# Kernel optimization log

Measured on AMD Instinct MI355X. Metric: run time of the kernel, lower is better.

The kernel has to match this reference:

```python
import jax, jax.numpy as jnp
import numpy as np

N = 50000      # nodes
E = 800000     # edges
F_IN = 500     # input features
H = 128        # hidden_channels
C = 10         # classes


def setup_inputs() -> dict:
    key = jax.random.key(0)
    ks = jax.random.split(key, 9)
    x = jax.random.normal(ks[0], (N, F_IN), dtype=jnp.float32)
    edge_index = jax.random.randint(ks[1], (2, E), 0, N, dtype=jnp.int32)
    W1 = jax.random.normal(ks[2], (F_IN, H), dtype=jnp.float32) * 0.05
    b1 = jnp.zeros((H,), dtype=jnp.float32)
    W2 = jax.random.normal(ks[3], (H, H), dtype=jnp.float32) * 0.05
    b2 = jnp.zeros((H,), dtype=jnp.float32)
    Wo = jax.random.normal(ks[4], (H, C), dtype=jnp.float32) * 0.05
    bo = jnp.zeros((C,), dtype=jnp.float32)
    return {"x": x, "edge_index": edge_index, "W1": W1, "b1": b1,
            "W2": W2, "b2": b2, "Wo": Wo, "bo": bo}


def _gcn_conv(x, src, dst, norm, W, b):
    # x: [N, F] -> [N, out]; PyG GCNConv: transform, then normalized scatter-add
    h = x @ W                                    # [N, out]
    msg = h[src] * norm[:, None]                 # [E+N, out] gathered messages
    agg = jax.ops.segment_sum(msg, dst, num_segments=N)
    return agg + b


def reference(x, edge_index, W1, b1, W2, b2, Wo, bo):
    loop = jnp.arange(N, dtype=edge_index.dtype)
    src = jnp.concatenate([edge_index[0], loop])  # add self-loops
    dst = jnp.concatenate([edge_index[1], loop])
    # symmetric normalization deg^-1/2 A_hat deg^-1/2 (deg counted at target)
    deg = jnp.zeros((N,), dtype=x.dtype).at[dst].add(1.0)
    dis = jnp.where(deg > 0, jax.lax.rsqrt(deg), 0.0)
    norm = dis[src] * dis[dst]

    h = jax.nn.relu(_gcn_conv(x, src, dst, norm, W1, b1))
    h = jax.nn.relu(_gcn_conv(h, src, dst, norm, W2, b2))
    # eval-mode: dropout is identity
    return jax.nn.softmax(h @ Wo + bo, axis=1)
```

## Files before the change

### kernel.cpp

```cpp
#include <hip/hip_runtime.h>
#include <hip/hip_bf16.h>
#include <stdint.h>

#define N_NODES 50000
#define N_EDGES 800000
#define F_IN    500
#define HID     128
#define NCLS    10

typedef __attribute__((ext_vector_type(8))) short bf16x8;
typedef __attribute__((ext_vector_type(4))) float f32x4;


__global__ __launch_bounds__(256) void count_deg_k(const int* dst, int* cnt) {
    int e = blockIdx.x * 256 + threadIdx.x;
    if (e < N_EDGES) atomicAdd(&cnt[dst[e]], 1);
}

__global__ __launch_bounds__(256) void compute_dis_k(const int* cnt, float* dis) {
    int i = blockIdx.x * 256 + threadIdx.x;
    if (i < N_NODES) {
        float deg = (float)(cnt[i] + 1);
        dis[i] = rsqrtf(deg);
    }
}

__global__ __launch_bounds__(1024) void scan_k(const int* __restrict__ cnt, int* __restrict__ off) {
    __shared__ int part[1024];
    const int PER = 52;
    int tid = threadIdx.x;
    int base = tid * PER;
    int vals[PER];
    #pragma unroll
    for (int i = 0; i < PER; i += 4) {
        int idx = base + i;
        int4 v = make_int4(0, 0, 0, 0);
        if (idx + 3 < N_NODES) {
            v = *(const int4*)&cnt[idx];
        } else {
            if (idx + 0 < N_NODES) v.x = cnt[idx + 0];
            if (idx + 1 < N_NODES) v.y = cnt[idx + 1];
            if (idx + 2 < N_NODES) v.z = cnt[idx + 2];
            if (idx + 3 < N_NODES) v.w = cnt[idx + 3];
        }
        vals[i + 0] = v.x; vals[i + 1] = v.y; vals[i + 2] = v.z; vals[i + 3] = v.w;
    }
    int s = 0;
    #pragma unroll
    for (int i = 0; i < PER; ++i) s += vals[i];
    part[tid] = s;
    __syncthreads();
    for (int o = 1; o < 1024; o <<= 1) {
        int v = (tid >= o) ? part[tid - o] : 0;
        __syncthreads();
        part[tid] += v;
        __syncthreads();
    }
    int run = part[tid] - s;
    #pragma unroll
    for (int i = 0; i < PER; ++i) {
        int idx = base + i;
        if (idx < N_NODES) { off[idx] = run; run += vals[i]; }
    }
    if (tid == 1023) off[N_NODES] = N_EDGES;
}

__global__ __launch_bounds__(256) void fill_csr_k(const int* src, const int* dst,
                                                  const int* off, int* cur, int* csr) {
    int e = blockIdx.x * 256 + threadIdx.x;
    if (e < N_EDGES) {
        int d = dst[e];
        int p = off[d] + atomicAdd(&cur[d], 1);
        csr[p] = src[e];
    }
}


__global__ __launch_bounds__(256) void transpose_cast_k(const float* __restrict__ W,
                                                        __hip_bfloat16* __restrict__ WT,
                                                        int K, int KPAD) {
    int id = blockIdx.x * 256 + threadIdx.x;
    if (id >= 128 * KPAD) return;
    int n = id / KPAD;
    int k = id - n * KPAD;
    WT[id] = (k < K) ? __float2bfloat16(W[(long)k * 128 + n]) : __float2bfloat16(0.f);
}


template<int KPAD, int KREAL>
__global__ __launch_bounds__(256) void gemm_mfma_k(const float* __restrict__ A,
                                                   const __hip_bfloat16* __restrict__ BT,
                                                   float* __restrict__ Out, int M) {
    __shared__ __hip_bfloat16 As[64][72];
    __shared__ __hip_bfloat16 Bs[128][72];
    const int tid  = threadIdx.x;
    const int row0 = blockIdx.x * 64;
    const int wid  = tid >> 6, lane = tid & 63;
    const int wr   = (wid >> 1) * 32;
    const int wc   = (wid & 1) * 64;
    const int l15  = lane & 15;
    const int lk   = (lane >> 4) * 8;

    f32x4 acc[2][4];
    #pragma unroll
    for (int i = 0; i < 2; ++i)
        #pragma unroll
        for (int j = 0; j < 4; ++j) acc[i][j] = (f32x4){0.f, 0.f, 0.f, 0.f};

    const int arow = tid >> 2;
    const int aseg = (tid & 3) * 16;
    const int brow = tid >> 1;
    const int bseg = (tid & 1) * 32;
    const bool rowok = (row0 + arow) < M;
    const float* aptr = A + (long)(row0 + arow) * KREAL;

    for (int k0 = 0; k0 < KPAD; k0 += 64) {
        {
            float v[16];
            const float* ap = aptr + k0 + aseg;
            if (rowok && (k0 + aseg + 16 <= KREAL)) {
                #pragma unroll
                for (int i = 0; i < 4; ++i) {
                    float4 f = ((const float4*)ap)[i];
                    v[i*4+0] = f.x; v[i*4+1] = f.y; v[i*4+2] = f.z; v[i*4+3] = f.w;
                }
            } else {
                #pragma unroll
                for (int i = 0; i < 16; ++i) {
                    int gk = k0 + aseg + i;
                    v[i] = (rowok && gk < KREAL) ? ap[i] : 0.f;
                }
            }
            __hip_bfloat16 bb[16];
            #pragma unroll
            for (int i = 0; i < 16; ++i) bb[i] = __float2bfloat16(v[i]);
            *(bf16x8*)&As[arow][aseg]     = *(bf16x8*)&bb[0];
            *(bf16x8*)&As[arow][aseg + 8] = *(bf16x8*)&bb[8];
        }
        {
            const __hip_bfloat16* bp = BT + (long)brow * KPAD + k0 + bseg;
            #pragma unroll
            for (int i = 0; i < 4; ++i)
                *(bf16x8*)&Bs[brow][bseg + i * 8] = ((const bf16x8*)bp)[i];
        }
        __syncthreads();
        #pragma unroll
        for (int kk = 0; kk < 64; kk += 32) {
            bf16x8 af[2], bfr[4];
            #pragma unroll
            for (int i = 0; i < 2; ++i)
                af[i] = *(const bf16x8*)&As[wr + i * 16 + l15][kk + lk];
            #pragma unroll
            for (int j = 0; j < 4; ++j)
                bfr[j] = *(const bf16x8*)&Bs[wc + j * 16 + l15][kk + lk];
            #pragma unroll
            for (int i = 0; i < 2; ++i)
                #pragma unroll
                for (int j = 0; j < 4; ++j)
                    acc[i][j] = __builtin_amdgcn_mfma_f32_16x16x32_bf16(af[i], bfr[j], acc[i][j], 0, 0, 0);
        }
        __syncthreads();
    }
    const int r4 = (lane >> 4) * 4;
    #pragma unroll
    for (int i = 0; i < 2; ++i) {
        #pragma unroll
        for (int r = 0; r < 4; ++r) {
            int grow = row0 + wr + i * 16 + r4 + r;
            if (grow < M) {
                float* op = Out + (long)grow * 128 + wc + l15;
                #pragma unroll
                for (int j = 0; j < 4; ++j) op[j * 16] = acc[i][j][r];
            }
        }
    }
}


__global__ __launch_bounds__(256) void agg_k(const float* __restrict__ Hin,
                                             float* __restrict__ Hout,
                                             const int* __restrict__ off,
                                             const int* __restrict__ csr,
                                             const float* __restrict__ dis,
                                             const float* __restrict__ bias) {
    int w = (blockIdx.x * 256 + threadIdx.x) >> 6;
    int lane = threadIdx.x & 63;
    if (w >= N_NODES) return;
    int n = w;
    int e0 = off[n], e1 = off[n + 1];
    float dn = dis[n];

    const float2* hn = (const float2*)(Hin + (long)n * HID);
    float2 hv = hn[lane];
    float sw = dn * dn;
    float ax = hv.x * sw, ay = hv.y * sw;

    int e = e0;
    for (; e + 4 <= e1; e += 4) {
        int s0 = csr[e + 0], s1 = csr[e + 1], s2 = csr[e + 2], s3 = csr[e + 3];
        float w0 = dis[s0] * dn, w1 = dis[s1] * dn, w2 = dis[s2] * dn, w3 = dis[s3] * dn;
        float2 m0 = ((const float2*)(Hin + (long)s0 * HID))[lane];
        float2 m1 = ((const float2*)(Hin + (long)s1 * HID))[lane];
        float2 m2 = ((const float2*)(Hin + (long)s2 * HID))[lane];
        float2 m3 = ((const float2*)(Hin + (long)s3 * HID))[lane];
        ax = fmaf(m0.x, w0, ax); ay = fmaf(m0.y, w0, ay);
        ax = fmaf(m1.x, w1, ax); ay = fmaf(m1.y, w1, ay);
        ax = fmaf(m2.x, w2, ax); ay = fmaf(m2.y, w2, ay);
        ax = fmaf(m3.x, w3, ax); ay = fmaf(m3.y, w3, ay);
    }
    for (; e < e1; ++e) {
        int s = csr[e];
        float wgt = dis[s] * dn;
        float2 m = ((const float2*)(Hin + (long)s * HID))[lane];
        ax = fmaf(m.x, wgt, ax);
        ay = fmaf(m.y, wgt, ay);
    }
    float2 bv = ((const float2*)bias)[lane];
    float ox = ax + bv.x, oy = ay + bv.y;
    ox = ox > 0.f ? ox : 0.f;
    oy = oy > 0.f ? oy : 0.f;
    ((float2*)(Hout + (long)n * HID))[lane] = make_float2(ox, oy);
}


__global__ __launch_bounds__(256) void head_k(const float* __restrict__ Hf,
                                              const float* __restrict__ Wo,
                                              const float* __restrict__ bo,
                                              float* __restrict__ out) {
    __shared__ float wsh[HID * NCLS];
    __shared__ float bsh[NCLS];
    int tid = threadIdx.x;
    for (int i = tid; i < HID * NCLS; i += 256) wsh[i] = Wo[i];
    if (tid < NCLS) bsh[tid] = bo[tid];
    __syncthreads();

    int w = (blockIdx.x * 256 + tid) >> 6;
    int lane = tid & 63;
    if (w >= N_NODES) return;

    float h0 = Hf[(long)w * HID + lane];
    float h1 = Hf[(long)w * HID + 64 + lane];

    float logit[NCLS];
    #pragma unroll
    for (int c = 0; c < NCLS; ++c) {
        float p = h0 * wsh[lane * NCLS + c] + h1 * wsh[(lane + 64) * NCLS + c];
        #pragma unroll
        for (int o = 32; o > 0; o >>= 1) p += __shfl_xor(p, o);
        logit[c] = p + bsh[c];
    }
    if (lane == 0) {
        float m = logit[0];
        #pragma unroll
        for (int c = 1; c < NCLS; ++c) m = fmaxf(m, logit[c]);
        float es[NCLS]; float ssum = 0.f;
        #pragma unroll
        for (int c = 0; c < NCLS; ++c) { es[c] = __expf(logit[c] - m); ssum += es[c]; }
        float inv = 1.f / ssum;
        #pragma unroll
        for (int c = 0; c < NCLS; ++c) out[(long)w * NCLS + c] = es[c] * inv;
    }
}


static inline char* align256(char* p) {
    return (char*)(((uintptr_t)p + 255) & ~(uintptr_t)255);
}

extern "C" void kernel_launch(void* const* d_in, const int* in_sizes, int n_in,
                              void* d_out, int out_size, void* d_ws, size_t ws_size,
                              hipStream_t stream) {
    const float* x   = (const float*)d_in[0];
    const int*   ei  = (const int*)d_in[1];
    const float* W1  = (const float*)d_in[2];
    const float* b1  = (const float*)d_in[3];
    const float* W2  = (const float*)d_in[4];
    const float* b2  = (const float*)d_in[5];
    const float* Wo  = (const float*)d_in[6];
    const float* bo  = (const float*)d_in[7];
    float* out = (float*)d_out;

    const int* srcp = ei;
    const int* dstp = ei + N_EDGES;

    char* wsb = (char*)d_ws;
    float* hA = (float*)align256(wsb);                 wsb = (char*)(hA + (size_t)N_NODES * HID);
    float* hB = (float*)align256(wsb);                 wsb = (char*)(hB + (size_t)N_NODES * HID);
    __hip_bfloat16* W1T = (__hip_bfloat16*)align256(wsb); wsb = (char*)(W1T + 128 * 512);
    __hip_bfloat16* W2T = (__hip_bfloat16*)align256(wsb); wsb = (char*)(W2T + 128 * 128);
    int*   cnt = (int*)align256(wsb);                  wsb = (char*)(cnt + N_NODES);
    int*   off = (int*)align256(wsb);                  wsb = (char*)(off + N_NODES + 1);
    int*   cur = (int*)align256(wsb);                  wsb = (char*)(cur + N_NODES);
    int*   csr = (int*)align256(wsb);                  wsb = (char*)(csr + N_EDGES);
    float* dis = (float*)align256(wsb);                wsb = (char*)(dis + N_NODES);

    hipMemsetAsync(cnt, 0, sizeof(int) * N_NODES, stream);
    hipMemsetAsync(cur, 0, sizeof(int) * N_NODES, stream);

    int ebl = (N_EDGES + 255) / 256;
    int nbl = (N_NODES + 255) / 256;
    count_deg_k<<<ebl, 256, 0, stream>>>(dstp, cnt);
    compute_dis_k<<<nbl, 256, 0, stream>>>(cnt, dis);
    scan_k<<<1, 1024, 0, stream>>>(cnt, off);
    fill_csr_k<<<ebl, 256, 0, stream>>>(srcp, dstp, off, cur, csr);

    transpose_cast_k<<<(128 * 512 + 255) / 256, 256, 0, stream>>>(W1, W1T, 500, 512);
    transpose_cast_k<<<(128 * 128 + 255) / 256, 256, 0, stream>>>(W2, W2T, 128, 128);

    int gblocks = (N_NODES + 63) / 64;
    int wblocks = (N_NODES + 3) / 4;

    gemm_mfma_k<512, 500><<<gblocks, 256, 0, stream>>>(x, W1T, hA, N_NODES);
    agg_k<<<wblocks, 256, 0, stream>>>(hA, hB, off, csr, dis, b1);
    gemm_mfma_k<128, 128><<<gblocks, 256, 0, stream>>>(hB, W2T, hA, N_NODES);
    agg_k<<<wblocks, 256, 0, stream>>>(hA, hB, off, csr, dis, b2);
    head_k<<<wblocks, 256, 0, stream>>>(hB, Wo, bo, out);
}
```

Measured before the change: 469.8 us.

## Store hidden features in bf16, fuse head into aggregation, merge setup kernels

Intermediate node features are now stored as bf16 instead of fp32, which halves the gather traffic in the aggregation kernels and the GEMM output and input traffic. The second aggregation is fused with the output head and softmax, removing one kernel and one feature round trip. Setup is condensed: the degree rsqrt is folded into the scan, the CSR fill reuses the count array by decrementing it, and both weight transposes run in one launch. The GEMM gains register prefetch of the next tile and writes its output through LDS as coalesced bf16 rows. The cost is extra bf16 rounding error on the intermediate features.

```diff
diff --git a/kernel.cpp b/kernel.cpp
--- a/kernel.cpp
+++ b/kernel.cpp
@@ -11,21 +11,22 @@
 typedef __attribute__((ext_vector_type(8))) short bf16x8;
 typedef __attribute__((ext_vector_type(4))) float f32x4;
 
-
-__global__ __launch_bounds__(256) void count_deg_k(const int* dst, int* cnt) {
+__device__ __forceinline__ float bf_lo(uint32_t u) { return __uint_as_float(u << 16); }
+__device__ __forceinline__ float bf_hi(uint32_t u) { return __uint_as_float(u & 0xffff0000u); }
+__device__ __forceinline__ uint32_t bf_pack(float a, float b) {
+    __hip_bfloat162 t; t.x = __float2bfloat16(a); t.y = __float2bfloat16(b);
+    uint32_t r; __builtin_memcpy(&r, &t, 4); return r;
+}
+
+
+__global__ __launch_bounds__(256) void count_deg_k(const int* __restrict__ dst, int* __restrict__ cnt) {
     int e = blockIdx.x * 256 + threadIdx.x;
     if (e < N_EDGES) atomicAdd(&cnt[dst[e]], 1);
 }
 
-__global__ __launch_bounds__(256) void compute_dis_k(const int* cnt, float* dis) {
-    int i = blockIdx.x * 256 + threadIdx.x;
-    if (i < N_NODES) {
-        float deg = (float)(cnt[i] + 1);
-        dis[i] = rsqrtf(deg);
-    }
-}
-
-__global__ __launch_bounds__(1024) void scan_k(const int* __restrict__ cnt, int* __restrict__ off) {
+__global__ __launch_bounds__(1024) void scan_dis_k(const int* __restrict__ cnt,
+                                                   int* __restrict__ off,
+                                                   float* __restrict__ dis) {
     __shared__ int part[1024];
     const int PER = 52;
     int tid = threadIdx.x;
@@ -60,39 +61,54 @@
     #pragma unroll
     for (int i = 0; i < PER; ++i) {
         int idx = base + i;
-        if (idx < N_NODES) { off[idx] = run; run += vals[i]; }
+        if (idx < N_NODES) {
+            off[idx] = run; run += vals[i];
+            dis[idx] = rsqrtf((float)(vals[i] + 1));
+        }
     }
     if (tid == 1023) off[N_NODES] = N_EDGES;
 }
 
-__global__ __launch_bounds__(256) void fill_csr_k(const int* src, const int* dst,
-                                                  const int* off, int* cur, int* csr) {
+__global__ __launch_bounds__(256) void fill_csr_k(const int* __restrict__ src,
+                                                  const int* __restrict__ dst,
+                                                  const int* __restrict__ off,
+                                                  int* __restrict__ cnt,
+                                                  int* __restrict__ csr) {
     int e = blockIdx.x * 256 + threadIdx.x;
     if (e < N_EDGES) {
         int d = dst[e];
-        int p = off[d] + atomicAdd(&cur[d], 1);
-        csr[p] = src[e];
-    }
-}
-
-
-__global__ __launch_bounds__(256) void transpose_cast_k(const float* __restrict__ W,
-                                                        __hip_bfloat16* __restrict__ WT,
-                                                        int K, int KPAD) {
+        int old = atomicAdd(&cnt[d], -1);
+        csr[off[d] + old - 1] = src[e];
+    }
+}
+
+
+__global__ __launch_bounds__(256) void transpose_both_k(const float* __restrict__ W1,
+                                                        const float* __restrict__ W2,
+                                                        __hip_bfloat16* __restrict__ W1T,
+                                                        __hip_bfloat16* __restrict__ W2T) {
     int id = blockIdx.x * 256 + threadIdx.x;
-    if (id >= 128 * KPAD) return;
-    int n = id / KPAD;
-    int k = id - n * KPAD;
-    WT[id] = (k < K) ? __float2bfloat16(W[(long)k * 128 + n]) : __float2bfloat16(0.f);
-}
-
-
-template<int KPAD, int KREAL>
-__global__ __launch_bounds__(256) void gemm_mfma_k(const float* __restrict__ A,
+    if (id < 128 * 512) {
+        int n = id >> 9, k = id & 511;
+        W1T[id] = (k < F_IN) ? __float2bfloat16(W1[(long)k * 128 + n]) : __float2bfloat16(0.f);
+    } else {
+        int id2 = id - 128 * 512;
+        if (id2 < 128 * 128) {
+            int n = id2 >> 7, k = id2 & 127;
+            W2T[id2] = __float2bfloat16(W2[(long)k * 128 + n]);
+        }
+    }
+}
+
+
+template<int KPAD, int KREAL, bool AF32>
+__global__ __launch_bounds__(256) void gemm_mfma_k(const void* __restrict__ Av,
                                                    const __hip_bfloat16* __restrict__ BT,
-                                                   float* __restrict__ Out, int M) {
-    __shared__ __hip_bfloat16 As[64][72];
-    __shared__ __hip_bfloat16 Bs[128][72];
+                                                   __hip_bfloat16* __restrict__ Out, int M) {
+    __shared__ __hip_bfloat16 smem[64 * 72 + 128 * 72];
+    auto As = (__hip_bfloat16 (*)[72])smem;
+    auto Bs = (__hip_bfloat16 (*)[72])(smem + 64 * 72);
+
     const int tid  = threadIdx.x;
     const int row0 = blockIdx.x * 64;
     const int wid  = tid >> 6, lane = tid & 63;
@@ -112,17 +128,18 @@
     const int brow = tid >> 1;
     const int bseg = (tid & 1) * 32;
     const bool rowok = (row0 + arow) < M;
-    const float* aptr = A + (long)(row0 + arow) * KREAL;
-
-    for (int k0 = 0; k0 < KPAD; k0 += 64) {
-        {
+
+    bf16x8 a0, a1, b0, b1, b2v, b3;
+
+    auto loadA = [&](int k0, bf16x8& r0, bf16x8& r1) {
+        if (AF32) {
+            const float* ap = (const float*)Av + (size_t)(row0 + arow) * KREAL + k0 + aseg;
             float v[16];
-            const float* ap = aptr + k0 + aseg;
             if (rowok && (k0 + aseg + 16 <= KREAL)) {
                 #pragma unroll
                 for (int i = 0; i < 4; ++i) {
                     float4 f = ((const float4*)ap)[i];
-                    v[i*4+0] = f.x; v[i*4+1] = f.y; v[i*4+2] = f.z; v[i*4+3] = f.w;
+                    v[4*i] = f.x; v[4*i+1] = f.y; v[4*i+2] = f.z; v[4*i+3] = f.w;
                 }
             } else {
                 #pragma unroll
@@ -134,16 +151,34 @@
             __hip_bfloat16 bb[16];
             #pragma unroll
             for (int i = 0; i < 16; ++i) bb[i] = __float2bfloat16(v[i]);
-            *(bf16x8*)&As[arow][aseg]     = *(bf16x8*)&bb[0];
-            *(bf16x8*)&As[arow][aseg + 8] = *(bf16x8*)&bb[8];
-        }
-        {
-            const __hip_bfloat16* bp = BT + (long)brow * KPAD + k0 + bseg;
-            #pragma unroll
-            for (int i = 0; i < 4; ++i)
-                *(bf16x8*)&Bs[brow][bseg + i * 8] = ((const bf16x8*)bp)[i];
-        }
+            r0 = *(bf16x8*)&bb[0]; r1 = *(bf16x8*)&bb[8];
+        } else {
+            const __hip_bfloat16* ap = (const __hip_bfloat16*)Av + (size_t)(row0 + arow) * KREAL + k0 + aseg;
+            if (rowok) { r0 = ((const bf16x8*)ap)[0]; r1 = ((const bf16x8*)ap)[1]; }
+            else       { r0 = (bf16x8)(short)0;       r1 = (bf16x8)(short)0; }
+        }
+    };
+    auto loadB = [&](int k0, bf16x8& r0, bf16x8& r1, bf16x8& r2, bf16x8& r3) {
+        const __hip_bfloat16* bp = BT + (size_t)brow * KPAD + k0 + bseg;
+        r0 = ((const bf16x8*)bp)[0]; r1 = ((const bf16x8*)bp)[1];
+        r2 = ((const bf16x8*)bp)[2]; r3 = ((const bf16x8*)bp)[3];
+    };
+
+    loadA(0, a0, a1);
+    loadB(0, b0, b1, b2v, b3);
+    const int NT = KPAD / 64;
+    for (int t = 0; t < NT; ++t) {
+        *(bf16x8*)&As[arow][aseg]      = a0;
+        *(bf16x8*)&As[arow][aseg + 8]  = a1;
+        *(bf16x8*)&Bs[brow][bseg]      = b0;
+        *(bf16x8*)&Bs[brow][bseg + 8]  = b1;
+        *(bf16x8*)&Bs[brow][bseg + 16] = b2v;
+        *(bf16x8*)&Bs[brow][bseg + 24] = b3;
         __syncthreads();
+        if (t + 1 < NT) {
+            loadA((t + 1) * 64, a0, a1);
+            loadB((t + 1) * 64, b0, b1, b2v, b3);
+        }
         #pragma unroll
         for (int kk = 0; kk < 64; kk += 32) {
             bf16x8 af[2], bfr[4];
@@ -161,72 +196,78 @@
         }
         __syncthreads();
     }
+
+    auto Cs = (__hip_bfloat16 (*)[136])smem;
     const int r4 = (lane >> 4) * 4;
     #pragma unroll
-    for (int i = 0; i < 2; ++i) {
-        #pragma unroll
-        for (int r = 0; r < 4; ++r) {
-            int grow = row0 + wr + i * 16 + r4 + r;
-            if (grow < M) {
-                float* op = Out + (long)grow * 128 + wc + l15;
-                #pragma unroll
-                for (int j = 0; j < 4; ++j) op[j * 16] = acc[i][j][r];
-            }
-        }
-    }
-}
-
-
-__global__ __launch_bounds__(256) void agg_k(const float* __restrict__ Hin,
-                                             float* __restrict__ Hout,
-                                             const int* __restrict__ off,
-                                             const int* __restrict__ csr,
-                                             const float* __restrict__ dis,
-                                             const float* __restrict__ bias) {
+    for (int i = 0; i < 2; ++i)
+        #pragma unroll
+        for (int j = 0; j < 4; ++j)
+            #pragma unroll
+            for (int r = 0; r < 4; ++r)
+                Cs[wr + i * 16 + r4 + r][wc + j * 16 + l15] = __float2bfloat16(acc[i][j][r]);
+    __syncthreads();
+    int trow = tid >> 2, tseg = (tid & 3) * 32;
+    if (row0 + trow < M) {
+        bf16x8* op = (bf16x8*)(Out + (size_t)(row0 + trow) * 128 + tseg);
+        #pragma unroll
+        for (int s = 0; s < 4; ++s) op[s] = *(bf16x8*)&Cs[trow][tseg + 8 * s];
+    }
+}
+
+
+__global__ __launch_bounds__(256) void agg_bf16_k(const __hip_bfloat16* __restrict__ Hin,
+                                                  __hip_bfloat16* __restrict__ Hout,
+                                                  const int* __restrict__ off,
+                                                  const int* __restrict__ csr,
+                                                  const float* __restrict__ dis,
+                                                  const float* __restrict__ bias) {
     int w = (blockIdx.x * 256 + threadIdx.x) >> 6;
     int lane = threadIdx.x & 63;
     if (w >= N_NODES) return;
-    int n = w;
-    int e0 = off[n], e1 = off[n + 1];
-    float dn = dis[n];
-
-    const float2* hn = (const float2*)(Hin + (long)n * HID);
-    float2 hv = hn[lane];
+    int e0 = off[w], e1 = off[w + 1];
+    float dn = dis[w];
+    const uint32_t* hrow = (const uint32_t*)Hin;
+
+    uint32_t u = hrow[(size_t)w * 64 + lane];
     float sw = dn * dn;
-    float ax = hv.x * sw, ay = hv.y * sw;
+    float ax = bf_lo(u) * sw, ay = bf_hi(u) * sw;
 
     int e = e0;
     for (; e + 4 <= e1; e += 4) {
-        int s0 = csr[e + 0], s1 = csr[e + 1], s2 = csr[e + 2], s3 = csr[e + 3];
+        int s0 = csr[e], s1 = csr[e + 1], s2 = csr[e + 2], s3 = csr[e + 3];
         float w0 = dis[s0] * dn, w1 = dis[s1] * dn, w2 = dis[s2] * dn, w3 = dis[s3] * dn;
-        float2 m0 = ((const float2*)(Hin + (long)s0 * HID))[lane];
-        float2 m1 = ((const float2*)(Hin + (long)s1 * HID))[lane];
-        float2 m2 = ((const float2*)(Hin + (long)s2 * HID))[lane];
-        float2 m3 = ((const float2*)(Hin + (long)s3 * HID))[lane];
-        ax = fmaf(m0.x, w0, ax); ay = fmaf(m0.y, w0, ay);
-        ax = fmaf(m1.x, w1, ax); ay = fmaf(m1.y, w1, ay);
-        ax = fmaf(m2.x, w2, ax); ay = fmaf(m2.y, w2, ay);
-        ax = fmaf(m3.x, w3, ax); ay = fmaf(m3.y, w3, ay);
+        uint32_t m0 = hrow[(size_t)s0 * 64 + lane];
+        uint32_t m1 = hrow[(size_t)s1 * 64 + lane];
+        uint32_t m2 = hrow[(size_t)s2 * 64 + lane];
+        uint32_t m3 = hrow[(size_t)s3 * 64 + lane];
+        ax = fmaf(bf_lo(m0), w0, ax); ay = fmaf(bf_hi(m0), w0, ay);
+        ax = fmaf(bf_lo(m1), w1, ax); ay = fmaf(bf_hi(m1), w1, ay);
+        ax = fmaf(bf_lo(m2), w2, ax); ay = fmaf(bf_hi(m2), w2, ay);
+        ax = fmaf(bf_lo(m3), w3, ax); ay = fmaf(bf_hi(m3), w3, ay);
     }
     for (; e < e1; ++e) {
         int s = csr[e];
         float wgt = dis[s] * dn;
-        float2 m = ((const float2*)(Hin + (long)s * HID))[lane];
-        ax = fmaf(m.x, wgt, ax);
-        ay = fmaf(m.y, wgt, ay);
+        uint32_t m = hrow[(size_t)s * 64 + lane];
+        ax = fmaf(bf_lo(m), wgt, ax);
+        ay = fmaf(bf_hi(m), wgt, ay);
     }
     float2 bv = ((const float2*)bias)[lane];
-    float ox = ax + bv.x, oy = ay + bv.y;
-    ox = ox > 0.f ? ox : 0.f;
-    oy = oy > 0.f ? oy : 0.f;
-    ((float2*)(Hout + (long)n * HID))[lane] = make_float2(ox, oy);
-}
-
-
-__global__ __launch_bounds__(256) void head_k(const float* __restrict__ Hf,
-                                              const float* __restrict__ Wo,
-                                              const float* __restrict__ bo,
-                                              float* __restrict__ out) {
+    float ox = fmaxf(ax + bv.x, 0.f);
+    float oy = fmaxf(ay + bv.y, 0.f);
+    ((uint32_t*)Hout)[(size_t)w * 64 + lane] = bf_pack(ox, oy);
+}
+
+
+__global__ __launch_bounds__(256) void agg_head_k(const __hip_bfloat16* __restrict__ Hin,
+                                                  const int* __restrict__ off,
+                                                  const int* __restrict__ csr,
+                                                  const float* __restrict__ dis,
+                                                  const float* __restrict__ b2,
+                                                  const float* __restrict__ Wo,
+                                                  const float* __restrict__ bo,
+                                                  float* __restrict__ out) {
     __shared__ float wsh[HID * NCLS];
     __shared__ float bsh[NCLS];
     int tid = threadIdx.x;
@@ -238,27 +279,63 @@
     int lane = tid & 63;
     if (w >= N_NODES) return;
 
-    float h0 = Hf[(long)w * HID + lane];
-    float h1 = Hf[(long)w * HID + 64 + lane];
-
-    float logit[NCLS];
+    float wreg0[NCLS], wreg1[NCLS];
     #pragma unroll
     for (int c = 0; c < NCLS; ++c) {
-        float p = h0 * wsh[lane * NCLS + c] + h1 * wsh[(lane + 64) * NCLS + c];
+        wreg0[c] = wsh[(2 * lane) * NCLS + c];
+        wreg1[c] = wsh[(2 * lane + 1) * NCLS + c];
+    }
+
+    int e0 = off[w], e1 = off[w + 1];
+    float dn = dis[w];
+    const uint32_t* hrow = (const uint32_t*)Hin;
+
+    uint32_t u = hrow[(size_t)w * 64 + lane];
+    float sw = dn * dn;
+    float ax = bf_lo(u) * sw, ay = bf_hi(u) * sw;
+
+    int e = e0;
+    for (; e + 4 <= e1; e += 4) {
+        int s0 = csr[e], s1 = csr[e + 1], s2 = csr[e + 2], s3 = csr[e + 3];
+        float w0 = dis[s0] * dn, w1 = dis[s1] * dn, w2 = dis[s2] * dn, w3 = dis[s3] * dn;
+        uint32_t m0 = hrow[(size_t)s0 * 64 + lane];
+        uint32_t m1 = hrow[(size_t)s1 * 64 + lane];
+        uint32_t m2 = hrow[(size_t)s2 * 64 + lane];
+        uint32_t m3 = hrow[(size_t)s3 * 64 + lane];
+        ax = fmaf(bf_lo(m0), w0, ax); ay = fmaf(bf_hi(m0), w0, ay);
+        ax = fmaf(bf_lo(m1), w1, ax); ay = fmaf(bf_hi(m1), w1, ay);
+        ax = fmaf(bf_lo(m2), w2, ax); ay = fmaf(bf_hi(m2), w2, ay);
+        ax = fmaf(bf_lo(m3), w3, ax); ay = fmaf(bf_hi(m3), w3, ay);
+    }
+    for (; e < e1; ++e) {
+        int s = csr[e];
+        float wgt = dis[s] * dn;
+        uint32_t m = hrow[(size_t)s * 64 + lane];
+        ax = fmaf(bf_lo(m), wgt, ax);
+        ay = fmaf(bf_hi(m), wgt, ay);
+    }
+    float2 bv = ((const float2*)b2)[lane];
+    float hx = fmaxf(ax + bv.x, 0.f);
+    float hy = fmaxf(ay + bv.y, 0.f);
+
+    float l[NCLS];
+    #pragma unroll
+    for (int c = 0; c < NCLS; ++c) {
+        float p = fmaf(hx, wreg0[c], hy * wreg1[c]);
         #pragma unroll
         for (int o = 32; o > 0; o >>= 1) p += __shfl_xor(p, o);
-        logit[c] = p + bsh[c];
+        l[c] = p + bsh[c];
     }
     if (lane == 0) {
-        float m = logit[0];
-        #pragma unroll
-        for (int c = 1; c < NCLS; ++c) m = fmaxf(m, logit[c]);
+        float m = l[0];
+        #pragma unroll
+        for (int c = 1; c < NCLS; ++c) m = fmaxf(m, l[c]);
         float es[NCLS]; float ssum = 0.f;
         #pragma unroll
-        for (int c = 0; c < NCLS; ++c) { es[c] = __expf(logit[c] - m); ssum += es[c]; }
+        for (int c = 0; c < NCLS; ++c) { es[c] = __expf(l[c] - m); ssum += es[c]; }
         float inv = 1.f / ssum;
         #pragma unroll
-        for (int c = 0; c < NCLS; ++c) out[(long)w * NCLS + c] = es[c] * inv;
+        for (int c = 0; c < NCLS; ++c) out[(size_t)w * NCLS + c] = es[c] * inv;
     }
 }
 
@@ -284,35 +361,28 @@
     const int* dstp = ei + N_EDGES;
 
     char* wsb = (char*)d_ws;
-    float* hA = (float*)align256(wsb);                 wsb = (char*)(hA + (size_t)N_NODES * HID);
-    float* hB = (float*)align256(wsb);                 wsb = (char*)(hB + (size_t)N_NODES * HID);
+    __hip_bfloat16* hA = (__hip_bfloat16*)align256(wsb);  wsb = (char*)(hA + (size_t)N_NODES * HID);
+    __hip_bfloat16* hB = (__hip_bfloat16*)align256(wsb);  wsb = (char*)(hB + (size_t)N_NODES * HID);
     __hip_bfloat16* W1T = (__hip_bfloat16*)align256(wsb); wsb = (char*)(W1T + 128 * 512);
     __hip_bfloat16* W2T = (__hip_bfloat16*)align256(wsb); wsb = (char*)(W2T + 128 * 128);
-    int*   cnt = (int*)align256(wsb);                  wsb = (char*)(cnt + N_NODES);
-    int*   off = (int*)align256(wsb);                  wsb = (char*)(off + N_NODES + 1);
-    int*   cur = (int*)align256(wsb);                  wsb = (char*)(cur + N_NODES);
-    int*   csr = (int*)align256(wsb);                  wsb = (char*)(csr + N_EDGES);
-    float* dis = (float*)align256(wsb);                wsb = (char*)(dis + N_NODES);
+    int*   cnt = (int*)align256(wsb);                     wsb = (char*)(cnt + N_NODES);
+    int*   off = (int*)align256(wsb);                     wsb = (char*)(off + N_NODES + 1);
+    int*   csr = (int*)align256(wsb);                     wsb = (char*)(csr + N_EDGES);
+    float* dis = (float*)align256(wsb);                   wsb = (char*)(dis + N_NODES);
 
     hipMemsetAsync(cnt, 0, sizeof(int) * N_NODES, stream);
-    hipMemsetAsync(cur, 0, sizeof(int) * N_NODES, stream);
 
     int ebl = (N_EDGES + 255) / 256;
-    int nbl = (N_NODES + 255) / 256;
     count_deg_k<<<ebl, 256, 0, stream>>>(dstp, cnt);
-    compute_dis_k<<<nbl, 256, 0, stream>>>(cnt, dis);
-    scan_k<<<1, 1024, 0, stream>>>(cnt, off);
-    fill_csr_k<<<ebl, 256, 0, stream>>>(srcp, dstp, off, cur, csr);
-
-    transpose_cast_k<<<(128 * 512 + 255) / 256, 256, 0, stream>>>(W1, W1T, 500, 512);
-    transpose_cast_k<<<(128 * 128 + 255) / 256, 256, 0, stream>>>(W2, W2T, 128, 128);
+    scan_dis_k<<<1, 1024, 0, stream>>>(cnt, off, dis);
+    fill_csr_k<<<ebl, 256, 0, stream>>>(srcp, dstp, off, cnt, csr);
+    transpose_both_k<<<(128 * 512 + 128 * 128 + 255) / 256, 256, 0, stream>>>(W1, W2, W1T, W2T);
 
     int gblocks = (N_NODES + 63) / 64;
     int wblocks = (N_NODES + 3) / 4;
 
-    gemm_mfma_k<512, 500><<<gblocks, 256, 0, stream>>>(x, W1T, hA, N_NODES);
-    agg_k<<<wblocks, 256, 0, stream>>>(hA, hB, off, csr, dis, b1);
-    gemm_mfma_k<128, 128><<<gblocks, 256, 0, stream>>>(hB, W2T, hA, N_NODES);
-    agg_k<<<wblocks, 256, 0, stream>>>(hA, hB, off, csr, dis, b2);
-    head_k<<<wblocks, 256, 0, stream>>>(hB, Wo, bo, out);
-}
+    gemm_mfma_k<512, 500, true><<<gblocks, 256, 0, stream>>>(x, W1T, hA, N_NODES);
+    agg_bf16_k<<<wblocks, 256, 0, stream>>>(hA, hB, off, csr, dis, b1);
+    gemm_mfma_k<128, 128, false><<<gblocks, 256, 0, stream>>>(hB, W2T, hA, N_NODES);
+    agg_head_k<<<wblocks, 256, 0, stream>>>(hA, off, csr, dis, b2, Wo, bo, out);
+}
```

After: 442.0 us. 5.9% less time.
